# Optimization experiments

Hardware: AMD Instinct MI355X
Metric: run time of the kernel (lower is better)

Reference implementation:

```python
import jax, jax.numpy as jnp
import numpy as np

B, L, H = 8, 1024, 512
CHUNK = 16  # query-row chunk size for the score computation; L % CHUNK == 0


def setup_inputs() -> dict:
    key = jax.random.key(0)
    ks = jax.random.split(key, 6)
    s = 1.0 / np.sqrt(H)  # torch nn.Linear default init bound
    return {
        "inputs": jax.random.normal(ks[0], (B, L, H), jnp.float32),
        "W1": jax.random.uniform(ks[1], (H, H), jnp.float32, -s, s),
        "b1": jax.random.uniform(ks[2], (H,), jnp.float32, -s, s),
        "W2": jax.random.uniform(ks[3], (H, H), jnp.float32, -s, s),
        "b2": jax.random.uniform(ks[4], (H,), jnp.float32, -s, s),
        # torch: nn.init.normal_(q, mean=-0.02, std=0.02)
        "q": jax.random.normal(ks[5], (H,), jnp.float32) * 0.02 - 0.02,
    }


def _scores(u1, u2, q):
    # u[b,i,j] = tanh(u1[b,i,:] + u2[b,j,:]) . q  -- computed in row-chunks to
    # avoid materializing the full [B,L,L,H] tensor the torch loop implies.
    Bx, Lx, Hx = u1.shape
    n = Lx // CHUNK
    u1c = u1.reshape(Bx, n, CHUNK, Hx).transpose(1, 0, 2, 3)  # [n, B, c, H]

    def step(carry, u1_i):
        t = jnp.tanh(u1_i[:, :, None, :] + u2[:, None, :, :])  # [B, c, L, H]
        return carry, jnp.einsum('bclh,h->bcl', t, q)

    _, s = jax.lax.scan(jax.checkpoint(step), None, u1c)  # [n, B, c, L]
    return s.transpose(1, 0, 2, 3).reshape(Bx, Lx, Lx)


def reference(inputs, W1, b1, W2, b2, q):
    u1 = inputs @ W1.T + b1  # [B, L, H]
    u2 = inputs @ W2.T + b2  # [B, L, H]
    u = _scores(u1, u2, q)   # [B, L, L]
    # relu=False in init, so no relu on u
    a = jax.nn.softmax(u, axis=2)
    h = jnp.einsum('bij,bjh->bih', a, inputs)  # [B, L, H]
    return h, a
```

## Files before the change

### kernel.cpp

```cpp
#include <hip/hip_runtime.h>

typedef _Float16 f16;
typedef _Float16 f16x2 __attribute__((ext_vector_type(2)));
typedef _Float16 f16x4 __attribute__((ext_vector_type(4)));
typedef _Float16 f16x8 __attribute__((ext_vector_type(8)));
typedef float f32x4 __attribute__((ext_vector_type(4)));

#define LOG2E_X2 2.8853900817779268f

__constant__ float D8[8] = {0.543915f, 0.177997f, 0.0652351f, 0.0242575f,
                            0.00903807f, 0.00336823f, 0.00125536f, 0.000467884f};

static __device__ __forceinline__ void gl2lds16(const void* g, void* l) {
  __builtin_amdgcn_global_load_lds((const __attribute__((address_space(1))) void*)g,
                                   (__attribute__((address_space(3))) void*)l, 16, 0, 0);
}


__global__ __launch_bounds__(256) void k_prep_x(const float* __restrict__ X,
                                                f16* __restrict__ Xh, f16* __restrict__ XhT) {
  const int ht = blockIdx.x, it = blockIdx.y, b = blockIdx.z;
  __shared__ f16 Lt[64][72];
  const int t = threadIdx.x;
  const int r = t >> 4, c4 = (t & 15) * 4;
  const float* Xb = X + ((size_t)b * 1024 + it * 64) * 512 + ht * 64;
#pragma unroll
  for (int k = 0; k < 4; ++k) {
    const int rr = r + 16 * k;
    float4 v = *(const float4*)&Xb[(size_t)rr * 512 + c4];
    f16 h0 = (f16)v.x, h1 = (f16)v.y, h2 = (f16)v.z, h3 = (f16)v.w;
    *(f16x4*)&Xh[((size_t)b * 1024 + it * 64 + rr) * 512 + ht * 64 + c4] = {h0, h1, h2, h3};
    Lt[c4 + 0][rr] = h0; Lt[c4 + 1][rr] = h1; Lt[c4 + 2][rr] = h2; Lt[c4 + 3][rr] = h3;
  }
  __syncthreads();
  const int hr = t >> 2, seg = t & 3;
  f16* dst = &XhT[((size_t)b * 512 + ht * 64 + hr) * 1024 + it * 64 + seg * 16];
  *(f16x8*)(dst) = *(const f16x8*)&Lt[hr][seg * 16];
  *(f16x8*)(dst + 8) = *(const f16x8*)&Lt[hr][seg * 16 + 8];
}

__global__ __launch_bounds__(256) void k_prep_w(const float* __restrict__ W1,
                                                const float* __restrict__ W2,
                                                f16* __restrict__ Wh) {
  const int row = blockIdx.x, z = blockIdx.y, t = threadIdx.x;
  const float* W = z ? W2 : W1;
  float2 v = *(const float2*)&W[(size_t)row * 512 + t * 2];
  *(f16x2*)&Wh[(size_t)z * 262144 + (size_t)row * 512 + t * 2] = {(f16)v.x, (f16)v.y};
}

template <int NM>
__global__ __launch_bounds__(256) void k_trig(const float* __restrict__ u1,
                                              const float* __restrict__ u2,
                                              const float* __restrict__ q,
                                              f16* __restrict__ At, f16* __restrict__ Bt,
                                              float* __restrict__ qa, float* __restrict__ qb,
                                              int m0, int wq) {
  const int i = blockIdx.x, t = threadIdx.x;
  const float w = 0.62831853f;
  const float2 a2 = *(const float2*)&u1[(size_t)i * 512 + 2 * t];
  const float2 b2 = *(const float2*)&u2[(size_t)i * 512 + 2 * t];
  const float2 q2 = *(const float2*)&q[2 * t];
  if (wq) {
    float sa = q2.x * a2.x + q2.y * a2.y;
    float sb = q2.x * b2.x + q2.y * b2.y;
#pragma unroll
    for (int o = 1; o < 64; o <<= 1) { sa += __shfl_xor(sa, o); sb += __shfl_xor(sb, o); }
    __shared__ float red[8];
    const int lane = t & 63, widx = t >> 6;
    if (lane == 0) { red[widx] = sa; red[4 + widx] = sb; }
    __syncthreads();
    if (t == 0) qa[i] = red[0] + red[1] + red[2] + red[3];
    if (t == 1) qb[i] = red[4] + red[5] + red[6] + red[7];
  }
  float s1[4], c1[4], sm_[4], cm_[4];
  const float ang[4] = {w * a2.x, w * a2.y, w * b2.x, w * b2.y};
#pragma unroll
  for (int u = 0; u < 4; ++u) {
    __sincosf(ang[u], &s1[u], &c1[u]);
    if (m0 == 1) { sm_[u] = s1[u]; cm_[u] = c1[u]; }
    else __sincosf(m0 * ang[u], &sm_[u], &cm_[u]);
  }
  const size_t ldT = (size_t)NM * 1024;
  f16* Ar = At + (size_t)i * ldT + 2 * t;
  f16* Br = Bt + (size_t)i * ldT + 2 * t;
#pragma unroll
  for (int j = 0; j < NM; ++j) {
    const float dm = D8[m0 - 1 + j];
    const float qdx = q2.x * dm, qdy = q2.y * dm;
    *(f16x2*)(Ar + j * 1024)       = {(f16)(qdx * sm_[0]), (f16)(qdy * sm_[1])};
    *(f16x2*)(Ar + j * 1024 + 512) = {(f16)(qdx * cm_[0]), (f16)(qdy * cm_[1])};
    *(f16x2*)(Br + j * 1024)       = {(f16)cm_[2], (f16)cm_[3]};
    *(f16x2*)(Br + j * 1024 + 512) = {(f16)sm_[2], (f16)sm_[3]};
    if (j + 1 < NM) {
#pragma unroll
      for (int u = 0; u < 4; ++u) {
        const float ns = sm_[u] * c1[u] + cm_[u] * s1[u];
        const float nc = cm_[u] * c1[u] - sm_[u] * s1[u];
        sm_[u] = ns; cm_[u] = nc;
      }
    }
  }
}

template <int MODE, int ACC>
__global__ __launch_bounds__(512, 2) void k_gemm(
    const f16* __restrict__ A, const f16* __restrict__ B, float* __restrict__ C,
    const float* __restrict__ e0, const float* __restrict__ e1,
    int Kloop, int ldAB, long halfA, long halfC) {
  __shared__ alignas(16) char sm[2][2][256 * 64 * 2];
  const int t = threadIdx.x;
  const int nx = blockIdx.x, my = blockIdx.y, z = blockIdx.z;
  const f16* Ab; const f16* Bb; float* Cb; const float* bias = nullptr;
  int ldC;
  if (MODE == 0) {
    Ab = A + (size_t)my * 256 * ldAB;
    Bb = B + (size_t)z * 262144 + (size_t)nx * 256 * ldAB;
    Cb = C + (size_t)z * 4194304 + (size_t)my * 256 * 512 + nx * 256;
    bias = (z ? e1 : e0) + nx * 256;
    ldC = 512;
  } else if (MODE == 1) {
    const int b = z & 7, h = z >> 3;
    Ab = A + ((size_t)(b * 1024 + my * 256)) * ldAB + h * halfA;
    Bb = B + ((size_t)(b * 1024 + nx * 256)) * ldAB + h * halfA;
    Cb = C + h * halfC + ((size_t)(b * 1024 + my * 256)) * 1024 + nx * 256;
    ldC = 1024;
  } else {
    Ab = A + ((size_t)(z * 1024 + my * 256)) * ldAB;
    Bb = B + ((size_t)(z * 512 + nx * 256)) * ldAB;
    Cb = C + (size_t)z * 524288 + (size_t)my * 256 * 512 + nx * 256;
    ldC = 512;
  }
  const int wid = t >> 6, lane = t & 63;
  const int wr = wid >> 2, wc = wid & 3;
  const int rl = lane & 15, kc = lane >> 4;
  f32x4 acc[8][4] = {};

  auto stage = [&](int buf, int kt) {
    const f16* gA = Ab + kt * 64;
    const f16* gB = Bb + kt * 64;
    char* lA = sm[buf][0];
    char* lB = sm[buf][1];
#pragma unroll
    for (int ii = 0; ii < 4; ++ii) {
      const int lin = ii * 512 + t;
      const int row = lin >> 3, c = lin & 7;
      const size_t go = (size_t)row * ldAB + ((c ^ (row & 7)) * 8);
      gl2lds16(gA + go, lA + ii * 8192 + wid * 1024);
      gl2lds16(gB + go, lB + ii * 8192 + wid * 1024);
    }
  };

  const int nkt = Kloop >> 6;
  stage(0, 0);
  __syncthreads();
  for (int kt = 0; kt < nkt; ++kt) {
    const int cur = kt & 1;
    if (kt + 1 < nkt) stage(cur ^ 1, kt + 1);
    const char* lA = sm[cur][0];
    const char* lB = sm[cur][1];
#pragma unroll
    for (int kk = 0; kk < 2; ++kk) {
      f16x8 av[8], bv[4];
#pragma unroll
      for (int fi = 0; fi < 8; ++fi) {
        const int rloc = wr * 128 + fi * 16 + rl;
        av[fi] = *(const f16x8*)(lA + rloc * 128 + (((kc + 4 * kk) ^ (rloc & 7)) << 4));
      }
#pragma unroll
      for (int fj = 0; fj < 4; ++fj) {
        const int cloc = wc * 64 + fj * 16 + rl;
        bv[fj] = *(const f16x8*)(lB + cloc * 128 + (((kc + 4 * kk) ^ (cloc & 7)) << 4));
      }
#pragma unroll
      for (int fi = 0; fi < 8; ++fi)
#pragma unroll
        for (int fj = 0; fj < 4; ++fj)
          acc[fi][fj] = __builtin_amdgcn_mfma_f32_16x16x32_f16(av[fi], bv[fj], acc[fi][fj], 0, 0, 0);
    }
    __syncthreads();
  }
#pragma unroll
  for (int fj = 0; fj < 4; ++fj) {
    const int gcol = wc * 64 + fj * 16 + rl;
    const float bvv = (MODE == 0) ? bias[gcol] : 0.f;
#pragma unroll
    for (int fi = 0; fi < 8; ++fi) {
      const int grow0 = wr * 128 + fi * 16 + kc * 4;
      f32x4 v = acc[fi][fj];
#pragma unroll
      for (int r = 0; r < 4; ++r) {
        const size_t o = (size_t)(grow0 + r) * ldC + gcol;
        float x = v[r] + bvv;
        if (ACC) x += Cb[o];
        Cb[o] = x;
      }
    }
  }
}

__global__ __launch_bounds__(256) void k_softmax2(const float* __restrict__ P0,
                                                  const float* __restrict__ P1,
                                                  const float* __restrict__ qa,
                                                  const float* __restrict__ qb,
                                                  float* __restrict__ out_a,
                                                  f16* __restrict__ a16) {
  const int row = blockIdx.x, t = threadIdx.x;
  const int b = row >> 10;
  const size_t off = (size_t)row * 1024 + t * 4;
  float4 p0 = *(const float4*)(P0 + off);
  float4 p1 = *(const float4*)(P1 + off);
  float4 qb4 = *(const float4*)(qb + (size_t)b * 1024 + t * 4);
  const float qi = qa[row];
  float4 v;
  v.x = p0.x + p1.x + 0.2f * (qi + qb4.x);
  v.y = p0.y + p1.y + 0.2f * (qi + qb4.y);
  v.z = p0.z + p1.z + 0.2f * (qi + qb4.z);
  v.w = p0.w + p1.w + 0.2f * (qi + qb4.w);
  float m = fmaxf(fmaxf(v.x, v.y), fmaxf(v.z, v.w));
#pragma unroll
  for (int o = 1; o < 64; o <<= 1) m = fmaxf(m, __shfl_xor(m, o));
  __shared__ float red[4];
  const int w = t >> 6, ln = t & 63;
  if (ln == 0) red[w] = m;
  __syncthreads();
  m = fmaxf(fmaxf(red[0], red[1]), fmaxf(red[2], red[3]));
  v.x = __expf(v.x - m); v.y = __expf(v.y - m);
  v.z = __expf(v.z - m); v.w = __expf(v.w - m);
  float s = v.x + v.y + v.z + v.w;
#pragma unroll
  for (int o = 1; o < 64; o <<= 1) s += __shfl_xor(s, o);
  __syncthreads();
  if (ln == 0) red[w] = s;
  __syncthreads();
  s = red[0] + red[1] + red[2] + red[3];
  const float inv = 1.0f / s;
  v.x *= inv; v.y *= inv; v.z *= inv; v.w *= inv;
  *(float4*)(out_a + off) = v;
  *(f16x4*)(a16 + off) = {(f16)v.x, (f16)v.y, (f16)v.z, (f16)v.w};
}

typedef short s16x2 __attribute__((ext_vector_type(2)));

static __device__ __forceinline__ float fdot2f(f16x2 a, f16x2 b, float c) {
#if __has_builtin(__builtin_amdgcn_fdot2)
  return __builtin_amdgcn_fdot2(a, b, c, false);
#else
  return c + (float)a[0] * (float)b[0] + (float)a[1] * (float)b[1];
#endif
}

__global__ void k_qprep(const float* __restrict__ q, f16* __restrict__ qh,
                        float* __restrict__ qsum) {
  const int t = threadIdx.x;
  float v = q[t];
  qh[t] = (f16)v;
  float s = v;
#pragma unroll
  for (int o = 1; o < 64; o <<= 1) s += __shfl_xor(s, o);
  __shared__ float red[8];
  if ((t & 63) == 0) red[t >> 6] = s;
  __syncthreads();
  if (t == 0) {
    float tot = 0.f;
#pragma unroll
    for (int i = 0; i < 8; ++i) tot += red[i];
    *qsum = tot;
  }
}

__global__ __launch_bounds__(256) void k_gemm_exp(
    const float* __restrict__ X, const float* __restrict__ W1,
    const float* __restrict__ b1, const float* __restrict__ W2,
    const float* __restrict__ b2, f16* __restrict__ e1, f16* __restrict__ e2) {
  const int z = blockIdx.z;
  const float* W = z ? W2 : W1;
  const float* bias = z ? b2 : b1;
  f16* out = z ? e2 : e1;
  const int r0 = blockIdx.y * 64;
  const int c0 = blockIdx.x * 64;
  __shared__ alignas(16) float Xs[64][68];
  __shared__ alignas(16) float Ws[64][68];
  const int t = threadIdx.x;
  const int row = t >> 2, seg = t & 3;
  const int tr = t >> 4, tc = t & 15;
  float acc[4][4] = {};
#pragma unroll 1
  for (int k0 = 0; k0 < 512; k0 += 64) {
    const float4* gx = (const float4*)(X + (size_t)(r0 + row) * 512 + k0 + seg * 16);
    float4* lx = (float4*)(&Xs[row][seg * 16]);
    lx[0] = gx[0]; lx[1] = gx[1]; lx[2] = gx[2]; lx[3] = gx[3];
    const float4* gw = (const float4*)(W + (size_t)(c0 + row) * 512 + k0 + seg * 16);
    float4* lw = (float4*)(&Ws[row][seg * 16]);
    lw[0] = gw[0]; lw[1] = gw[1]; lw[2] = gw[2]; lw[3] = gw[3];
    __syncthreads();
#pragma unroll 4
    for (int kk = 0; kk < 64; kk += 4) {
      float4 av[4], bv[4];
#pragma unroll
      for (int ii = 0; ii < 4; ++ii) av[ii] = *(const float4*)&Xs[tr + 16 * ii][kk];
#pragma unroll
      for (int jj = 0; jj < 4; ++jj) bv[jj] = *(const float4*)&Ws[tc + 16 * jj][kk];
#pragma unroll
      for (int ii = 0; ii < 4; ++ii) {
#pragma unroll
        for (int jj = 0; jj < 4; ++jj) {
          acc[ii][jj] = fmaf(av[ii].x, bv[jj].x, acc[ii][jj]);
          acc[ii][jj] = fmaf(av[ii].y, bv[jj].y, acc[ii][jj]);
          acc[ii][jj] = fmaf(av[ii].z, bv[jj].z, acc[ii][jj]);
          acc[ii][jj] = fmaf(av[ii].w, bv[jj].w, acc[ii][jj]);
        }
      }
    }
    __syncthreads();
  }
#pragma unroll
  for (int ii = 0; ii < 4; ++ii) {
    const int r = r0 + tr + 16 * ii;
#pragma unroll
    for (int jj = 0; jj < 4; ++jj) {
      const int c = c0 + tc + 16 * jj;
      float u = acc[ii][jj] + bias[c];
      float val = u * LOG2E_X2 - 4.0f;
      val = fminf(6.6759f, fmaxf(-14.6759f, val));
      out[(size_t)r * 512 + c] = (f16)exp2f(val);
    }
  }
}

template <int P>
static __device__ __forceinline__ void tanh_dot_step(const f16x8 (&Av)[4],
                                                     const f16x8 (&Bv)[4],
                                                     const f16x8& Qv, float (&acc)[4][4],
                                                     int c256, int kmag, int two2) {
  f16x2 qp = __builtin_shufflevector(Qv, Qv, 2 * P, 2 * P + 1);
#pragma unroll
  for (int jj = 0; jj < 4; ++jj) {
    f16x2 bp = __builtin_shufflevector(Bv[jj], Bv[jj], 2 * P, 2 * P + 1);
#pragma unroll
    for (int ii = 0; ii < 4; ++ii) {
      f16x2 ap = __builtin_shufflevector(Av[ii], Av[ii], 2 * P, 2 * P + 1);
      f16x2 d, r, tt;
      asm("v_pk_fma_f16 %0, %3, %4, %5\n\t"
          "v_pk_sub_i16 %1, %6, %0\n\t"
          "v_pk_fma_f16 %2, %0, %1, %7 neg_lo:[1,0,0] neg_hi:[1,0,0]\n\t"
          "v_pk_mul_f16 %1, %1, %2\n\t"
          "v_pk_fma_f16 %2, %0, %1, %7 neg_lo:[1,0,0] neg_hi:[1,0,0]\n\t"
          "v_pk_mul_f16 %1, %1, %2"
          : "=&v"(d), "=&v"(r), "=&v"(tt)
          : "v"(ap), "v"(bp), "v"(c256), "v"(kmag), "v"(two2));
      acc[ii][jj] = fdot2f(r, qp, acc[ii][jj]);
    }
  }
}

__global__ __launch_bounds__(256) void k_scores(const f16* __restrict__ e1,
                                                const f16* __restrict__ e2,
                                                const f16* __restrict__ qh,
                                                const float* __restrict__ qsum_p,
                                                float* __restrict__ out_a) {
  const int b = blockIdx.z, it = blockIdx.y, jt = blockIdx.x;
  __shared__ alignas(16) f16 As[64][72];
  __shared__ alignas(16) f16 Bs[64][72];
  __shared__ alignas(16) f16 Qs[512];
  const int t = threadIdx.x;
  const size_t eA = (size_t)(b * 1024 + it * 64) * 512;
  const size_t eB = (size_t)(b * 1024 + jt * 64) * 512;
  if (t < 64) ((uint4*)Qs)[t] = ((const uint4*)qh)[t];
  const int row = t >> 2, seg = t & 3;
  const int tr = t >> 4, tc = t & 15;
  const int c256 = 0x1C001C00;
  const int kmag = 0x77987798;
  const int two2 = 0x40004000;
  float acc[4][4] = {};
#pragma unroll 1
  for (int h0 = 0; h0 < 512; h0 += 64) {
    const f16* gA = e1 + eA + (size_t)row * 512 + h0;
    const f16* gB = e2 + eB + (size_t)row * 512 + h0;
    *(uint4*)(&As[row][seg * 8]) = *(const uint4*)(gA + seg * 8);
    *(uint4*)(&As[row][seg * 8 + 32]) = *(const uint4*)(gA + seg * 8 + 32);
    *(uint4*)(&Bs[row][seg * 8]) = *(const uint4*)(gB + seg * 8);
    *(uint4*)(&Bs[row][seg * 8 + 32]) = *(const uint4*)(gB + seg * 8 + 32);
    __syncthreads();
#pragma unroll 2
    for (int g = 0; g < 8; ++g) {
      f16x8 Av[4], Bv[4], Qv;
#pragma unroll
      for (int ii = 0; ii < 4; ++ii) Av[ii] = *(const f16x8*)&As[tr + 16 * ii][g * 8];
#pragma unroll
      for (int jj = 0; jj < 4; ++jj) Bv[jj] = *(const f16x8*)&Bs[tc + 16 * jj][g * 8];
      Qv = *(const f16x8*)&Qs[h0 + g * 8];
      tanh_dot_step<0>(Av, Bv, Qv, acc, c256, kmag, two2);
      tanh_dot_step<1>(Av, Bv, Qv, acc, c256, kmag, two2);
      tanh_dot_step<2>(Av, Bv, Qv, acc, c256, kmag, two2);
      tanh_dot_step<3>(Av, Bv, Qv, acc, c256, kmag, two2);
    }
    __syncthreads();
  }
  const float qs = *qsum_p;
#pragma unroll
  for (int ii = 0; ii < 4; ++ii) {
    const size_t orow = (size_t)(b * 1024 + it * 64 + tr + 16 * ii) * 1024;
#pragma unroll
    for (int jj = 0; jj < 4; ++jj)
      out_a[orow + jt * 64 + tc + 16 * jj] = qs - acc[ii][jj] * (1.0f / 128.0f);
  }
}

__global__ __launch_bounds__(256) void k_softmax(float* __restrict__ a) {
  float* row = a + (size_t)blockIdx.x * 1024;
  const int t = threadIdx.x;
  float4 v = ((const float4*)row)[t];
  float m = fmaxf(fmaxf(v.x, v.y), fmaxf(v.z, v.w));
#pragma unroll
  for (int o = 1; o < 64; o <<= 1) m = fmaxf(m, __shfl_xor(m, o));
  __shared__ float red[4];
  const int w = t >> 6, ln = t & 63;
  if (ln == 0) red[w] = m;
  __syncthreads();
  m = fmaxf(fmaxf(red[0], red[1]), fmaxf(red[2], red[3]));
  v.x = __expf(v.x - m); v.y = __expf(v.y - m);
  v.z = __expf(v.z - m); v.w = __expf(v.w - m);
  float s = v.x + v.y + v.z + v.w;
#pragma unroll
  for (int o = 1; o < 64; o <<= 1) s += __shfl_xor(s, o);
  __syncthreads();
  if (ln == 0) red[w] = s;
  __syncthreads();
  s = red[0] + red[1] + red[2] + red[3];
  const float inv = 1.0f / s;
  v.x *= inv; v.y *= inv; v.z *= inv; v.w *= inv;
  ((float4*)row)[t] = v;
}

__global__ __launch_bounds__(256) void k_av(const float* __restrict__ a,
                                            const float* __restrict__ X,
                                            float* __restrict__ h) {
  const int b = blockIdx.z;
  const int i0 = blockIdx.y * 64;
  const int c0 = blockIdx.x * 64;
  __shared__ alignas(16) float As[64][68];
  __shared__ alignas(16) float Xs[64][68];
  const float* Ab = a + (size_t)b * 1024 * 1024;
  const float* Xb = X + (size_t)b * 1024 * 512;
  const int t = threadIdx.x;
  const int row = t >> 2, seg = t & 3;
  const int tr = t >> 4, tc = t & 15;
  float acc[4][4] = {};
#pragma unroll 1
  for (int k0 = 0; k0 < 1024; k0 += 64) {
    const float4* ga = (const float4*)(Ab + (size_t)(i0 + row) * 1024 + k0 + seg * 16);
    float4* la = (float4*)(&As[row][seg * 16]);
    la[0] = ga[0]; la[1] = ga[1]; la[2] = ga[2]; la[3] = ga[3];
    const float4* gx = (const float4*)(Xb + (size_t)(k0 + row) * 512 + c0 + seg * 16);
    float4* lx = (float4*)(&Xs[row][seg * 16]);
    lx[0] = gx[0]; lx[1] = gx[1]; lx[2] = gx[2]; lx[3] = gx[3];
    __syncthreads();
#pragma unroll 8
    for (int k = 0; k < 64; ++k) {
      float av[4], bv[4];
#pragma unroll
      for (int ii = 0; ii < 4; ++ii) av[ii] = As[tr + 16 * ii][k];
#pragma unroll
      for (int jj = 0; jj < 4; ++jj) bv[jj] = Xs[k][tc + 16 * jj];
#pragma unroll
      for (int ii = 0; ii < 4; ++ii) {
#pragma unroll
        for (int jj = 0; jj < 4; ++jj)
          acc[ii][jj] = fmaf(av[ii], bv[jj], acc[ii][jj]);
      }
    }
    __syncthreads();
  }
#pragma unroll
  for (int ii = 0; ii < 4; ++ii) {
    const size_t orow = (size_t)b * 1024 * 512 + (size_t)(i0 + tr + 16 * ii) * 512;
#pragma unroll
    for (int jj = 0; jj < 4; ++jj)
      h[orow + c0 + tc + 16 * jj] = acc[ii][jj];
  }
}

extern "C" void kernel_launch(void* const* d_in, const int* in_sizes, int n_in,
                              void* d_out, int out_size, void* d_ws, size_t ws_size,
                              hipStream_t stream) {
  const float* inputs = (const float*)d_in[0];
  const float* W1 = (const float*)d_in[1];
  const float* b1 = (const float*)d_in[2];
  const float* W2 = (const float*)d_in[3];
  const float* b2 = (const float*)d_in[4];
  const float* q = (const float*)d_in[5];

  float* out_h = (float*)d_out;
  float* out_a = out_h + 4194304;

  const size_t FIXED = 101777408ULL;
  const size_t PER_M = 33554432ULL;
  if (ws_size < FIXED + PER_M) {
    char* ws = (char*)d_ws;
    f16* e1 = (f16*)ws;
    f16* e2 = (f16*)(ws + 8388608);
    f16* qh = (f16*)(ws + 16777216);
    float* qsum = (float*)(ws + 16778240);
    k_qprep<<<1, 512, 0, stream>>>(q, qh, qsum);
    k_gemm_exp<<<dim3(8, 128, 2), 256, 0, stream>>>(inputs, W1, b1, W2, b2, e1, e2);
    k_scores<<<dim3(16, 16, 8), 256, 0, stream>>>(e1, e2, qh, qsum, out_a);
    k_softmax<<<8192, 256, 0, stream>>>(out_a);
    k_av<<<dim3(8, 16, 8), 256, 0, stream>>>(out_a, inputs, out_h);
    return;
  }

  int nm = 8;
  while (FIXED + (size_t)nm * PER_M > ws_size) nm >>= 1;

  char* p = (char*)d_ws;
  f16* Xh = (f16*)p;            p += 8388608;
  f16* XhT = (f16*)p;           p += 8388608;
  f16* Wh = (f16*)p;            p += 1048576;
  f16* a16 = (f16*)p;           p += 16777216;
  float* qa = (float*)p;        p += 32768;
  float* qb = (float*)p;        p += 32768;
  float* P0 = (float*)p;        p += 33554432;
  float* P1 = (float*)p;        p += 33554432;
  f16* At = (f16*)p;            p += (size_t)nm * 16777216;
  f16* Bt = (f16*)p;

  float* u1 = out_a;
  float* u2 = out_a + 4194304;

  k_prep_x<<<dim3(8, 16, 8), 256, 0, stream>>>(inputs, Xh, XhT);
  k_prep_w<<<dim3(512, 2), 256, 0, stream>>>(W1, W2, Wh);
  k_gemm<0, 0><<<dim3(2, 32, 2), 512, 0, stream>>>(Xh, Wh, u1, b1, b2, 512, 512, 0, 0);

  const int chunks = 8 / nm;
  for (int cch = 0; cch < chunks; ++cch) {
    const int m0 = cch * nm + 1;
    switch (nm) {
      case 8: k_trig<8><<<8192, 256, 0, stream>>>(u1, u2, q, At, Bt, qa, qb, m0, cch == 0); break;
      case 4: k_trig<4><<<8192, 256, 0, stream>>>(u1, u2, q, At, Bt, qa, qb, m0, cch == 0); break;
      case 2: k_trig<2><<<8192, 256, 0, stream>>>(u1, u2, q, At, Bt, qa, qb, m0, cch == 0); break;
      default: k_trig<1><<<8192, 256, 0, stream>>>(u1, u2, q, At, Bt, qa, qb, m0, cch == 0); break;
    }
    const int Kloop = nm * 512;
    const int ldAB = nm * 1024;
    const long halfA = (long)nm * 512;
    if (cch == 0)
      k_gemm<1, 0><<<dim3(4, 4, 16), 512, 0, stream>>>(At, Bt, P0, nullptr, nullptr,
                                                       Kloop, ldAB, halfA, 8388608L);
    else
      k_gemm<1, 1><<<dim3(4, 4, 16), 512, 0, stream>>>(At, Bt, P0, nullptr, nullptr,
                                                       Kloop, ldAB, halfA, 8388608L);
  }

  k_softmax2<<<8192, 256, 0, stream>>>(P0, P1, qa, qb, out_a, a16);
  k_gemm<2, 0><<<dim3(2, 4, 8), 512, 0, stream>>>(a16, XhT, out_h, nullptr, nullptr,
                                                  1024, 1024, 0, 0);
}
```

Baseline: 298.6 us.

## Restructure GEMM main loop with prefetch-two pipeline and interleaved LDS reads/MFMA

The GEMM k-loop now issues two stages of global-to-LDS loads up front and uses explicit vmcnt waits plus raw barriers instead of __syncthreads. LDS fragment reads are split into quarters and interleaved with MFMA groups, using lgkmcnt waits, sched_barrier fences and s_setprio around the MFMA bursts. The aim is to overlap LDS reads and global loads with tensor math and keep register pressure bounded. Correctness now rests on hand-counted waitcnt values, so any miscount or compiler reordering risks races.

```diff
diff --git a/kernel.cpp b/kernel.cpp
--- a/kernel.cpp
+++ b/kernel.cpp
@@ -152,33 +152,68 @@
 
   const int nkt = Kloop >> 6;
   stage(0, 0);
-  __syncthreads();
+  if (nkt > 1) stage(1, 1);
+
   for (int kt = 0; kt < nkt; ++kt) {
-    const int cur = kt & 1;
-    if (kt + 1 < nkt) stage(cur ^ 1, kt + 1);
-    const char* lA = sm[cur][0];
-    const char* lB = sm[cur][1];
-#pragma unroll
-    for (int kk = 0; kk < 2; ++kk) {
-      f16x8 av[8], bv[4];
-#pragma unroll
-      for (int fi = 0; fi < 8; ++fi) {
-        const int rloc = wr * 128 + fi * 16 + rl;
-        av[fi] = *(const f16x8*)(lA + rloc * 128 + (((kc + 4 * kk) ^ (rloc & 7)) << 4));
-      }
-#pragma unroll
-      for (int fj = 0; fj < 4; ++fj) {
-        const int cloc = wc * 64 + fj * 16 + rl;
-        bv[fj] = *(const f16x8*)(lB + cloc * 128 + (((kc + 4 * kk) ^ (cloc & 7)) << 4));
-      }
-#pragma unroll
-      for (int fi = 0; fi < 8; ++fi)
-#pragma unroll
-        for (int fj = 0; fj < 4; ++fj)
-          acc[fi][fj] = __builtin_amdgcn_mfma_f32_16x16x32_f16(av[fi], bv[fj], acc[fi][fj], 0, 0, 0);
-    }
-    __syncthreads();
-  }
+    const char* lA = sm[kt & 1][0];
+    const char* lB = sm[kt & 1][1];
+
+    auto rdA = [&](f16x8 (&av)[4][2], int h) {
+#pragma unroll
+      for (int fi = 0; fi < 4; ++fi)
+#pragma unroll
+        for (int kk = 0; kk < 2; ++kk) {
+          const int rloc = wr * 128 + (h * 4 + fi) * 16 + rl;
+          av[fi][kk] = *(const f16x8*)(lA + rloc * 128 + (((kc + 4 * kk) ^ (rloc & 7)) << 4));
+        }
+    };
+    auto rdB = [&](f16x8 (&bv)[2][2], int p) {
+#pragma unroll
+      for (int fj = 0; fj < 2; ++fj)
+#pragma unroll
+        for (int kk = 0; kk < 2; ++kk) {
+          const int cloc = wc * 64 + (p * 2 + fj) * 16 + rl;
+          bv[fj][kk] = *(const f16x8*)(lB + cloc * 128 + (((kc + 4 * kk) ^ (cloc & 7)) << 4));
+        }
+    };
+    auto mma = [&](f16x8 (&av)[4][2], f16x8 (&bv)[2][2], int h, int p) {
+      __builtin_amdgcn_s_setprio(1);
+#pragma unroll
+      for (int kk = 0; kk < 2; ++kk)
+#pragma unroll
+        for (int fi = 0; fi < 4; ++fi)
+#pragma unroll
+          for (int fj = 0; fj < 2; ++fj)
+            acc[h * 4 + fi][p * 2 + fj] = __builtin_amdgcn_mfma_f32_16x16x32_f16(
+                av[fi][kk], bv[fj][kk], acc[h * 4 + fi][p * 2 + fj], 0, 0, 0);
+      __builtin_amdgcn_s_setprio(0);
+    };
+
+    if (kt + 1 < nkt) { asm volatile("s_waitcnt vmcnt(8)" ::: "memory"); }
+    else              { asm volatile("s_waitcnt vmcnt(0)" ::: "memory"); }
+    __builtin_amdgcn_s_barrier();
+    __builtin_amdgcn_sched_barrier(0);
+
+    f16x8 av0[4][2], av1[4][2], bv0[2][2], bv1[2][2];
+    rdA(av0, 0); rdB(bv0, 0);
+    rdB(bv1, 1);
+    asm volatile("s_waitcnt lgkmcnt(4)" ::: "memory");
+    __builtin_amdgcn_sched_barrier(0);
+    mma(av0, bv0, 0, 0);
+    rdA(av1, 1);
+    asm volatile("s_waitcnt lgkmcnt(8)" ::: "memory");
+    __builtin_amdgcn_sched_barrier(0);
+    mma(av0, bv1, 0, 1);
+    asm volatile("s_waitcnt lgkmcnt(0)" ::: "memory");
+    __builtin_amdgcn_sched_barrier(0);
+    mma(av1, bv1, 1, 1);
+    mma(av1, bv0, 1, 0);
+
+    asm volatile("s_waitcnt lgkmcnt(0)" ::: "memory");
+    __builtin_amdgcn_s_barrier();
+    if (kt + 2 < nkt) stage(kt & 1, kt + 2);
+  }
+
 #pragma unroll
   for (int fj = 0; fj < 4; ++fj) {
     const int gcol = wc * 64 + fj * 16 + rl;
```

After: 305.9 us. 1.02x slower.

## Remap GEMM blocks across XCDs and overlap next-tile loads with MFMA via vmcnt waits

Applied to the files above, without the earlier changes.

For the score GEMM (MODE 1), the launch becomes a flat 1D grid, and block indices are remapped so that the 4 column tiles sharing an A row-panel land on the same XCD, which should improve L2 reuse. In all GEMM modes, the main loop now issues the next tile's global-to-LDS loads and then waits with s_waitcnt vmcnt(8) plus a raw barrier, so only the current tile must have arrived. This replaces the full __syncthreads. MFMA sections are also raised to higher wave priority with s_setprio. The hand-written waitcnt counts rely on the exact number of outstanding loads, which is fragile if the compiler reorders memory operations.

```diff
diff --git a/kernel.cpp b/kernel.cpp
--- a/kernel.cpp
+++ b/kernel.cpp
@@ -109,7 +109,15 @@
     int Kloop, int ldAB, long halfA, long halfC) {
   __shared__ alignas(16) char sm[2][2][256 * 64 * 2];
   const int t = threadIdx.x;
-  const int nx = blockIdx.x, my = blockIdx.y, z = blockIdx.z;
+  int nx, my, z;
+  if (MODE == 1) {
+    const int lin = blockIdx.x;
+    const int xcd = lin & 7, s = lin >> 3;
+    const int g = xcd + 8 * (s >> 2);
+    nx = s & 3; my = g & 3; z = g >> 2;
+  } else {
+    nx = blockIdx.x; my = blockIdx.y; z = blockIdx.z;
+  }
   const f16* Ab; const f16* Bb; float* Cb; const float* bias = nullptr;
   int ldC;
   if (MODE == 0) {
@@ -142,8 +150,8 @@
     char* lB = sm[buf][1];
 #pragma unroll
     for (int ii = 0; ii < 4; ++ii) {
-      const int lin = ii * 512 + t;
-      const int row = lin >> 3, c = lin & 7;
+      const int lin2 = ii * 512 + t;
+      const int row = lin2 >> 3, c = lin2 & 7;
       const size_t go = (size_t)row * ldAB + ((c ^ (row & 7)) * 8);
       gl2lds16(gA + go, lA + ii * 8192 + wid * 1024);
       gl2lds16(gB + go, lB + ii * 8192 + wid * 1024);
@@ -152,12 +160,15 @@
 
   const int nkt = Kloop >> 6;
   stage(0, 0);
-  __syncthreads();
   for (int kt = 0; kt < nkt; ++kt) {
-    const int cur = kt & 1;
-    if (kt + 1 < nkt) stage(cur ^ 1, kt + 1);
-    const char* lA = sm[cur][0];
-    const char* lB = sm[cur][1];
+    if (kt + 1 < nkt) {
+      stage((kt + 1) & 1, kt + 1);
+      asm volatile("s_waitcnt vmcnt(8)\n\ts_barrier" ::: "memory");
+    } else {
+      asm volatile("s_waitcnt vmcnt(0)\n\ts_barrier" ::: "memory");
+    }
+    const char* lA = sm[kt & 1][0];
+    const char* lB = sm[kt & 1][1];
 #pragma unroll
     for (int kk = 0; kk < 2; ++kk) {
       f16x8 av[8], bv[4];
@@ -171,14 +182,17 @@
         const int cloc = wc * 64 + fj * 16 + rl;
         bv[fj] = *(const f16x8*)(lB + cloc * 128 + (((kc + 4 * kk) ^ (cloc & 7)) << 4));
       }
+      __builtin_amdgcn_s_setprio(1);
 #pragma unroll
       for (int fi = 0; fi < 8; ++fi)
 #pragma unroll
         for (int fj = 0; fj < 4; ++fj)
           acc[fi][fj] = __builtin_amdgcn_mfma_f32_16x16x32_f16(av[fi], bv[fj], acc[fi][fj], 0, 0, 0);
-    }
-    __syncthreads();
-  }
+      __builtin_amdgcn_s_setprio(0);
+    }
+    asm volatile("s_waitcnt lgkmcnt(0)\n\ts_barrier" ::: "memory");
+  }
+
 #pragma unroll
   for (int fj = 0; fj < 4; ++fj) {
     const int gcol = wc * 64 + fj * 16 + rl;
@@ -544,11 +558,11 @@
     const int ldAB = nm * 1024;
     const long halfA = (long)nm * 512;
     if (cch == 0)
-      k_gemm<1, 0><<<dim3(4, 4, 16), 512, 0, stream>>>(At, Bt, P0, nullptr, nullptr,
-                                                       Kloop, ldAB, halfA, 8388608L);
+      k_gemm<1, 0><<<dim3(256, 1, 1), 512, 0, stream>>>(At, Bt, P0, nullptr, nullptr,
+                                                        Kloop, ldAB, halfA, 8388608L);
     else
-      k_gemm<1, 1><<<dim3(4, 4, 16), 512, 0, stream>>>(At, Bt, P0, nullptr, nullptr,
-                                                       Kloop, ldAB, halfA, 8388608L);
+      k_gemm<1, 1><<<dim3(256, 1, 1), 512, 0, stream>>>(At, Bt, P0, nullptr, nullptr,
+                                                        Kloop, ldAB, halfA, 8388608L);
   }
 
   k_softmax2<<<8192, 256, 0, stream>>>(P0, P1, qa, qb, out_a, a16);
```

Result: no change. 299.4 us (+0.3%).

## Add dedicated pipelined score GEMM with half-tile staging and XCD-aware block mapping

Applied to the files above, without the earlier changes.

Replaces the generic MODE 1 GEMM used for the big score matmul with a dedicated kernel. It splits each 64-wide K tile into two halves that are staged asynchronously with global_load_lds while MFMAs run on the other half, and raises wave priority around the MFMA bursts. It also launches a 1D grid remapped so that tiles sharing A/B operands land on the same XCD for L2 reuse, and uses a k-major LDS layout without the XOR swizzle. The finer-grained barriers and hand-written waitcnts add synchronisation overhead and risk LDS bank conflicts or ordering bugs.

```diff
diff --git a/kernel.cpp b/kernel.cpp
--- a/kernel.cpp
+++ b/kernel.cpp
@@ -102,11 +102,129 @@
   }
 }
 
-template <int MODE, int ACC>
+template <int ACC>
+__global__ __launch_bounds__(512, 2) void k_gemm8(
+    const f16* __restrict__ A, const f16* __restrict__ B, float* __restrict__ C,
+    int Kloop, int ldAB, long halfA, long halfC) {
+  __shared__ alignas(16) char sm[4][32768];
+  const int t = threadIdx.x;
+  const int lin = blockIdx.x;
+  const int xcd = lin & 7, s = lin >> 3;
+  const int g = xcd + 8 * (s >> 2);
+  const int nx = s & 3, my = g & 3, z = g >> 2;
+  const int b = z & 7, h = z >> 3;
+  const f16* Ab = A + ((size_t)(b * 1024 + my * 256)) * ldAB + h * halfA;
+  const f16* Bb = B + ((size_t)(b * 1024 + nx * 256)) * ldAB + h * halfA;
+  float* Cb = C + h * halfC + ((size_t)(b * 1024 + my * 256)) * 1024 + nx * 256;
+
+  const int wid = t >> 6, lane = t & 63;
+  const int wr = wid >> 2, wc = wid & 3;
+  const int rl = lane & 15, kc = lane >> 4;
+  f32x4 acc[8][4] = {};
+
+  auto stageHalf = [&](int parity, int side, int hh, int kt2) {
+    const f16* gsrc = (side ? Bb : Ab) + kt2 * 64 + hh * 32;
+    char* ldst = &sm[parity * 2 + side][hh * 16384];
+#pragma unroll
+    for (int j = 0; j < 2; ++j) {
+      const int idx = j * 512 + t;
+      const int kl = idx >> 8, row = idx & 255;
+      gl2lds16(gsrc + (size_t)row * ldAB + kl * 8, ldst + idx * 16);
+    }
+  };
+  auto rdA = [&](f16x8 (&av)[4], int parity, int mh, int kk) {
+    const char* base = sm[parity * 2 + 0];
+#pragma unroll
+    for (int fi = 0; fi < 4; ++fi) {
+      const int row = wr * 128 + (mh * 4 + fi) * 16 + rl;
+      av[fi] = *(const f16x8*)(base + (kk * 4 + kc) * 4096 + row * 16);
+    }
+  };
+  auto rdB = [&](f16x8 (&bv)[4], int parity, int kk) {
+    const char* base = sm[parity * 2 + 1];
+#pragma unroll
+    for (int fj = 0; fj < 4; ++fj) {
+      const int col = wc * 64 + fj * 16 + rl;
+      bv[fj] = *(const f16x8*)(base + (kk * 4 + kc) * 4096 + col * 16);
+    }
+  };
+  auto mma16 = [&](f16x8 (&av)[4], f16x8 (&bv)[4], int mh) {
+    __builtin_amdgcn_s_setprio(1);
+#pragma unroll
+    for (int fi = 0; fi < 4; ++fi)
+#pragma unroll
+      for (int fj = 0; fj < 4; ++fj)
+        acc[mh * 4 + fi][fj] =
+            __builtin_amdgcn_mfma_f32_16x16x32_f16(av[fi], bv[fj], acc[mh * 4 + fi][fj], 0, 0, 0);
+    __builtin_amdgcn_s_setprio(0);
+  };
+
+  const int nkt = Kloop >> 6;
+  stageHalf(0, 0, 0, 0); stageHalf(0, 1, 0, 0);
+  stageHalf(0, 0, 1, 0); stageHalf(0, 1, 1, 0);
+  stageHalf(1, 0, 0, 1); stageHalf(1, 1, 0, 1);
+  asm volatile("s_waitcnt vmcnt(4)" ::: "memory");
+  __builtin_amdgcn_s_barrier();
+
+  for (int kt = 0; kt < nkt; ++kt) {
+    const int p = kt & 1, pn = p ^ 1;
+    f16x8 av[4], bv0[4], bv1[4];
+    rdA(av, p, 0, 0); rdB(bv0, p, 0);
+    if (kt + 1 < nkt) stageHalf(pn, 0, 1, kt + 1);
+    __builtin_amdgcn_s_barrier();
+    asm volatile("s_waitcnt lgkmcnt(0)" ::: "memory");
+    __builtin_amdgcn_sched_barrier(0);
+    mma16(av, bv0, 0);
+    __builtin_amdgcn_s_barrier();
+    rdA(av, p, 1, 0);
+    if (kt + 1 < nkt) stageHalf(pn, 1, 1, kt + 1);
+    __builtin_amdgcn_s_barrier();
+    asm volatile("s_waitcnt lgkmcnt(0)" ::: "memory");
+    __builtin_amdgcn_sched_barrier(0);
+    mma16(av, bv0, 1);
+    __builtin_amdgcn_s_barrier();
+    rdA(av, p, 0, 1); rdB(bv1, p, 1);
+    if (kt + 2 < nkt) stageHalf(p, 0, 0, kt + 2);
+    __builtin_amdgcn_s_barrier();
+    asm volatile("s_waitcnt lgkmcnt(0)" ::: "memory");
+    __builtin_amdgcn_sched_barrier(0);
+    mma16(av, bv1, 0);
+    __builtin_amdgcn_s_barrier();
+    rdA(av, p, 1, 1);
+    if (kt + 2 < nkt) stageHalf(p, 1, 0, kt + 2);
+    __builtin_amdgcn_s_barrier();
+    asm volatile("s_waitcnt lgkmcnt(0)" ::: "memory");
+    __builtin_amdgcn_sched_barrier(0);
+    mma16(av, bv1, 1);
+    if (kt + 1 < nkt) {
+      if (kt + 2 < nkt) asm volatile("s_waitcnt vmcnt(4)" ::: "memory");
+      else              asm volatile("s_waitcnt vmcnt(0)" ::: "memory");
+    }
+    __builtin_amdgcn_s_barrier();
+  }
+
+#pragma unroll
+  for (int fj = 0; fj < 4; ++fj) {
+    const int gcol = wc * 64 + fj * 16 + rl;
+#pragma unroll
+    for (int fi = 0; fi < 8; ++fi) {
+      const int grow0 = wr * 128 + fi * 16 + kc * 4;
+      f32x4 v = acc[fi][fj];
+#pragma unroll
+      for (int r = 0; r < 4; ++r) {
+        const size_t o = (size_t)(grow0 + r) * 1024 + gcol;
+        float x = v[r];
+        if (ACC) x += Cb[o];
+        Cb[o] = x;
+      }
+    }
+  }
+}
+
+template <int MODE>
 __global__ __launch_bounds__(512, 2) void k_gemm(
     const f16* __restrict__ A, const f16* __restrict__ B, float* __restrict__ C,
-    const float* __restrict__ e0, const float* __restrict__ e1,
-    int Kloop, int ldAB, long halfA, long halfC) {
+    const float* __restrict__ e0, const float* __restrict__ e1, int Kloop, int ldAB) {
   __shared__ alignas(16) char sm[2][2][256 * 64 * 2];
   const int t = threadIdx.x;
   const int nx = blockIdx.x, my = blockIdx.y, z = blockIdx.z;
@@ -118,12 +236,6 @@
     Cb = C + (size_t)z * 4194304 + (size_t)my * 256 * 512 + nx * 256;
     bias = (z ? e1 : e0) + nx * 256;
     ldC = 512;
-  } else if (MODE == 1) {
-    const int b = z & 7, h = z >> 3;
-    Ab = A + ((size_t)(b * 1024 + my * 256)) * ldAB + h * halfA;
-    Bb = B + ((size_t)(b * 1024 + nx * 256)) * ldAB + h * halfA;
-    Cb = C + h * halfC + ((size_t)(b * 1024 + my * 256)) * 1024 + nx * 256;
-    ldC = 1024;
   } else {
     Ab = A + ((size_t)(z * 1024 + my * 256)) * ldAB;
     Bb = B + ((size_t)(z * 512 + nx * 256)) * ldAB;
@@ -142,8 +254,8 @@
     char* lB = sm[buf][1];
 #pragma unroll
     for (int ii = 0; ii < 4; ++ii) {
-      const int lin = ii * 512 + t;
-      const int row = lin >> 3, c = lin & 7;
+      const int lin2 = ii * 512 + t;
+      const int row = lin2 >> 3, c = lin2 & 7;
       const size_t go = (size_t)row * ldAB + ((c ^ (row & 7)) * 8);
       gl2lds16(gA + go, lA + ii * 8192 + wid * 1024);
       gl2lds16(gB + go, lB + ii * 8192 + wid * 1024);
@@ -190,9 +302,7 @@
 #pragma unroll
       for (int r = 0; r < 4; ++r) {
         const size_t o = (size_t)(grow0 + r) * ldC + gcol;
-        float x = v[r] + bvv;
-        if (ACC) x += Cb[o];
-        Cb[o] = x;
+        Cb[o] = v[r] + bvv;
       }
     }
   }
@@ -529,7 +639,7 @@
 
   k_prep_x<<<dim3(8, 16, 8), 256, 0, stream>>>(inputs, Xh, XhT);
   k_prep_w<<<dim3(512, 2), 256, 0, stream>>>(W1, W2, Wh);
-  k_gemm<0, 0><<<dim3(2, 32, 2), 512, 0, stream>>>(Xh, Wh, u1, b1, b2, 512, 512, 0, 0);
+  k_gemm<0><<<dim3(2, 32, 2), 512, 0, stream>>>(Xh, Wh, u1, b1, b2, 512, 512);
 
   const int chunks = 8 / nm;
   for (int cch = 0; cch < chunks; ++cch) {
@@ -544,14 +654,11 @@
     const int ldAB = nm * 1024;
     const long halfA = (long)nm * 512;
     if (cch == 0)
-      k_gemm<1, 0><<<dim3(4, 4, 16), 512, 0, stream>>>(At, Bt, P0, nullptr, nullptr,
-                                                       Kloop, ldAB, halfA, 8388608L);
+      k_gemm8<0><<<dim3(256, 1, 1), 512, 0, stream>>>(At, Bt, P0, Kloop, ldAB, halfA, 8388608L);
     else
-      k_gemm<1, 1><<<dim3(4, 4, 16), 512, 0, stream>>>(At, Bt, P0, nullptr, nullptr,
-                                                       Kloop, ldAB, halfA, 8388608L);
+      k_gemm8<1><<<dim3(256, 1, 1), 512, 0, stream>>>(At, Bt, P0, Kloop, ldAB, halfA, 8388608L);
   }
 
   k_softmax2<<<8192, 256, 0, stream>>>(P0, P1, qa, qb, out_a, a16);
-  k_gemm<2, 0><<<dim3(2, 4, 8), 512, 0, stream>>>(a16, XhT, out_h, nullptr, nullptr,
-                                                  1024, 1024, 0, 0);
-}
+  k_gemm<2><<<dim3(2, 4, 8), 512, 0, stream>>>(a16, XhT, out_h, nullptr, nullptr, 1024, 1024);
+}
```

Measured after the change: 331.3 us. +10.9%, slower.
